# Kernel optimization log

Hardware: AMD Instinct MI355X
Metric: run time of the kernel (lower is better)

The kernel has to match this reference:

```python
import jax, jax.numpy as jnp
import numpy as np

LEVELS = 2
_H0 = jnp.array([0.0322231, -0.01260397, -0.09921954, 0.2978578,
                 0.80373875, 0.49761867, -0.02963553, -0.07576571], dtype=jnp.float32)
_H1 = _H0[::-1] * jnp.array([-1.0, 1.0] * 4, dtype=jnp.float32)  # db4 QMF


def subband_conv2d(x, kernel_2d, stride):
    # depthwise grouped conv: same 2D kernel applied to every channel
    C = x.shape[-1]
    k = jnp.tile(kernel_2d[:, :, None, None], (1, 1, 1, C))  # HWIO with I=1, groups=C
    return jax.lax.conv_general_dilated(
        x, k, window_strides=(stride, stride), padding='SAME',
        dimension_numbers=('NHWC', 'HWIO', 'NHWC'), feature_group_count=C)


def _upsample2d(t):
    B, H, W, C = t.shape
    return jnp.zeros((B, 2 * H, 2 * W, C), t.dtype).at[:, ::2, ::2, :].set(t)


def _local_conv(t, w):
    # per-spatial-position linear map over channels: [B,H,W,I] x [I,O,W,H] -> [B,H,W,O]
    return jnp.einsum('bhwi,iowh->bhwo', t, w)


def setup_inputs() -> dict:
    key = jax.random.key(0)
    ks = jax.random.split(key, 9)
    B, H, W, C, O = 16, 128, 128, 64, 64
    inp = {
        'x': jax.random.normal(ks[0], (B, H, W, C), dtype=jnp.float32),
        'wLL': 0.02 * jax.random.normal(ks[1], (C, O, 32, 32), dtype=jnp.float32),
        'wLH_l0': 0.02 * jax.random.normal(ks[2], (C, O, 64, 64), dtype=jnp.float32),
        'wHL_l0': 0.02 * jax.random.normal(ks[3], (C, O, 64, 64), dtype=jnp.float32),
        'wHH_l0': 0.02 * jax.random.normal(ks[4], (C, O, 64, 64), dtype=jnp.float32),
        'wLH_l1': 0.02 * jax.random.normal(ks[5], (C, O, 32, 32), dtype=jnp.float32),
        'wHL_l1': 0.02 * jax.random.normal(ks[6], (C, O, 32, 32), dtype=jnp.float32),
        'wHH_l1': 0.02 * jax.random.normal(ks[7], (C, O, 32, 32), dtype=jnp.float32),
    }
    return inp


def reference(x, wLL, wLH_l0, wHL_l0, wHH_l0, wLH_l1, wHL_l1, wHH_l1):
    h0, h1 = _H0, _H1
    g0, g1 = h0[::-1], h1[::-1]
    # H=W=128 is divisible by 2**levels, so no symmetric padding is needed.
    res = x
    details = []
    for _ in range(LEVELS):
        cLL = subband_conv2d(res, jnp.outer(h0, h0), 2)
        cLH = subband_conv2d(res, jnp.outer(h0, h1), 2)
        cHL = subband_conv2d(res, jnp.outer(h1, h0), 2)
        cHH = subband_conv2d(res, jnp.outer(h1, h1), 2)
        details.append((cLH, cHL, cHH))
        res = cLL
    yA = _local_conv(res, wLL)  # [B,32,32,O]
    det_w = [(wLH_l0, wHL_l0, wHH_l0), (wLH_l1, wHL_l1, wHH_l1)]
    td = []
    for i in range(LEVELS):
        lh, hl, hh = details[i]
        wlh, whl, whh = det_w[i]
        td.append((_local_conv(lh, wlh), _local_conv(hl, whl), _local_conv(hh, whh)))
    r = yA
    for i in reversed(range(LEVELS)):
        yLH, yHL, yHH = td[i]
        r = (subband_conv2d(_upsample2d(r), jnp.outer(g0, g0), 1)
             + subband_conv2d(_upsample2d(yLH), jnp.outer(g0, g1), 1)
             + subband_conv2d(_upsample2d(yHL), jnp.outer(g1, g0), 1)
             + subband_conv2d(_upsample2d(yHH), jnp.outer(g1, g1), 1))
    return r
```

## Files before the change

### kernel.cpp

```cpp
#include <hip/hip_runtime.h>

__device__ __constant__ float H0[8] = { 0.0322231f, -0.01260397f, -0.09921954f,  0.2978578f,
                                        0.80373875f, 0.49761867f, -0.02963553f, -0.07576571f};
__device__ __constant__ float H1[8] = { 0.07576571f, -0.02963553f, -0.49761867f, 0.80373875f,
                                       -0.2978578f, -0.09921954f,  0.01260397f,  0.0322231f};
__device__ __constant__ float G0[8] = {-0.07576571f, -0.02963553f,  0.49761867f, 0.80373875f,
                                        0.2978578f,  -0.09921954f, -0.01260397f, 0.0322231f};
__device__ __constant__ float G1[8] = { 0.0322231f,   0.01260397f, -0.09921954f, -0.2978578f,
                                        0.80373875f, -0.49761867f, -0.02963553f, 0.07576571f};

template<int HIN>
__global__ __launch_bounds__(256) void fwd_dwt(const float* __restrict__ in,
                                               float* __restrict__ oLL, float* __restrict__ oLH,
                                               float* __restrict__ oHL, float* __restrict__ oHH)
{
    constexpr int OH = HIN / 2;
    constexpr int TQ = OH / 2;
    const int tid = threadIdx.x;
    const int c = tid & 63;
    const int s = blockIdx.x * 4 + (tid >> 6);
    const int j = s % TQ;
    const int i = (s / TQ) % TQ;
    const int b = s / (TQ * TQ);

    float acc[2][2][4];
#pragma unroll
    for (int a = 0; a < 2; ++a)
#pragma unroll
        for (int d = 0; d < 2; ++d)
#pragma unroll
            for (int k = 0; k < 4; ++k) acc[a][d][k] = 0.f;

    const int iw0 = 4 * j - 3;
#pragma unroll
    for (int r = 0; r < 10; ++r) {
        const int ih = 4 * i + r - 3;
        if ((unsigned)ih < (unsigned)HIN) {
            const float* row = in + ((b * HIN + ih) * HIN) * 64 + c;
            float xv[10];
#pragma unroll
            for (int v = 0; v < 10; ++v) {
                const int iw = iw0 + v;
                xv[v] = ((unsigned)iw < (unsigned)HIN) ? row[iw * 64] : 0.f;
            }
            float h00 = 0.f, h01 = 0.f, h10 = 0.f, h11 = 0.f;
#pragma unroll
            for (int v = 0; v < 8; ++v) {
                h00 += H0[v] * xv[v];
                h10 += H1[v] * xv[v];
                h01 += H0[v] * xv[v + 2];
                h11 += H1[v] * xv[v + 2];
            }
#pragma unroll
            for (int ii = 0; ii < 2; ++ii) {
                const int u = r - 2 * ii;
                if (0 <= u && u < 8) {
                    const float a0 = H0[u], a1 = H1[u];
                    acc[ii][0][0] += a0 * h00;
                    acc[ii][0][1] += a0 * h10;
                    acc[ii][0][2] += a1 * h00;
                    acc[ii][0][3] += a1 * h10;
                    acc[ii][1][0] += a0 * h01;
                    acc[ii][1][1] += a0 * h11;
                    acc[ii][1][2] += a1 * h01;
                    acc[ii][1][3] += a1 * h11;
                }
            }
        }
    }

#pragma unroll
    for (int ii = 0; ii < 2; ++ii)
#pragma unroll
        for (int jj = 0; jj < 2; ++jj) {
            const int oh = 2 * i + ii, ow = 2 * j + jj;
            const int oidx = ((b * OH + oh) * OH + ow) * 64 + c;
            oLL[oidx] = acc[ii][jj][0];
            oLH[oidx] = acc[ii][jj][1];
            oHL[oidx] = acc[ii][jj][2];
            oHH[oidx] = acc[ii][jj][3];
        }
}

template<int HD>
__global__ __launch_bounds__(256) void act_tr(const float* __restrict__ in,
                                              float* __restrict__ outp)
{
    __shared__ float Ld[64][HD + 1];
    const int w = blockIdx.x;
    const int b = blockIdx.y;
    const int t = threadIdx.x;

    {
        const int i = t & 63;
        const int hq = t >> 6;
#pragma unroll
        for (int s = 0; s < HD / 4; ++s) {
            const int h = hq * (HD / 4) + s;
            Ld[i][h] = in[((size_t)(b * HD + h) * HD + w) * 64 + i];
        }
    }
    __syncthreads();
    {
        const int h = t & (HD - 1);
        const int iq = t / HD;
        constexpr int NIQ = 256 / HD;
#pragma unroll
        for (int s = 0; s < 64 / NIQ; ++s) {
            const int i = s * NIQ + iq;
            outp[((size_t)(w * 64 + i) * 16 + b) * HD + h] = Ld[i][h];
        }
    }
}

template<int HD, int OT>
__global__ __launch_bounds__(256) void local_conv_v8(
    const float* __restrict__ a0, const float* __restrict__ a1,
    const float* __restrict__ a2, const float* __restrict__ a3,
    const float* __restrict__ w0, const float* __restrict__ w1,
    const float* __restrict__ w2, const float* __restrict__ w3,
    float* __restrict__ o0, float* __restrict__ o1,
    float* __restrict__ o2, float* __restrict__ o3)
{
    constexpr int WH   = HD * HD;
    constexpr int HG   = HD / 32;
    constexpr int OGN  = 64 / OT;
    constexpr int PERZ = OGN * HD * HG;
    constexpr int NB   = 2;
    constexpr int NO4  = OT / 4;
    constexpr int NR   = 8;

    __shared__ float E[NB][32][NO4 * 4 + 4];

    const int nwg = gridDim.x;
    const int hb  = blockIdx.x;
    const int l   = (hb & 7) * (nwg >> 3) + (hb >> 3);

    const int z   = l / PERZ;
    int rem       = l - z * PERZ;
    const int w   = rem / (OGN * HG);
    rem          -= w * (OGN * HG);
    const int og  = rem / HG;
    const int hg  = rem - og * HG;
    const int hbase = hg * 32;

    const float* act = (z == 0) ? a0 : (z == 1) ? a1 : (z == 2) ? a2 : a3;
    const float* wgt = (z == 0) ? w0 : (z == 1) ? w1 : (z == 2) ? w2 : w3;
    float*       out = (z == 0) ? o0 : (z == 1) ? o1 : (z == 2) ? o2 : o3;

    const int t  = threadIdx.x;
    const int hc = t & 31;
    const int r  = t >> 5;
    const int b0 = r * NB;

    const float* wp = wgt + (size_t)(og * OT) * WH + w * HD + hbase + hc;
    const float* ap = act + ((size_t)(w * 64) * 16 + b0) * HD + hbase + hc;

    float acc[NB][OT];
#pragma unroll
    for (int j = 0; j < NB; ++j)
#pragma unroll
        for (int q = 0; q < OT; ++q) acc[j][q] = 0.f;

    for (int ch = 0; ch < 32; ++ch) {
        const int i0 = ch * 2;
        float wr[2][OT];
        float ar[2][NB];
#pragma unroll
        for (int ii = 0; ii < 2; ++ii) {
#pragma unroll
            for (int q = 0; q < OT; ++q)
                wr[ii][q] = wp[(size_t)((i0 + ii) * 64 + q) * WH];
#pragma unroll
            for (int j = 0; j < NB; ++j)
                ar[ii][j] = ap[(size_t)((i0 + ii) * 16 + j) * HD];
        }
#pragma unroll
        for (int ii = 0; ii < 2; ++ii)
#pragma unroll
            for (int j = 0; j < NB; ++j) {
                const float a = ar[ii][j];
#pragma unroll
                for (int q = 0; q < OT; ++q)
                    acc[j][q] += a * wr[ii][q];
            }
    }

    const int oF = t & (NO4 - 1);
    const int h2 = (t / NO4) & 31;
    const int be = t / (NO4 * 32);

    for (int p = 0; p < NR; ++p) {
        if (p) __syncthreads();
        if (r == p) {
#pragma unroll
            for (int j = 0; j < NB; ++j)
#pragma unroll
                for (int q = 0; q < OT; ++q)
                    E[j][hc][q] = acc[j][q];
        }
        __syncthreads();
        if (be < NB) {
            float4 v = *(const float4*)&E[be][h2][oF * 4];
            const int b = p * NB + be;
            *(float4*)(out + ((size_t)(b * HD + hbase + h2) * HD + w) * 64
                       + og * OT + oF * 4) = v;
        }
    }
}

template<int HOUT>
__global__ __launch_bounds__(256) void inv_dwt(const float* __restrict__ yLL,
                                               const float* __restrict__ yLH,
                                               const float* __restrict__ yHL,
                                               const float* __restrict__ yHH,
                                               float* __restrict__ out)
{
    constexpr int HS = HOUT / 2;
    const int tid = threadIdx.x;
    const int c = tid & 63;
    const int s = blockIdx.x * 4 + (tid >> 6);
    const int j = s % HS;
    const int i = (s / HS) % HS;
    const int b = s / (HS * HS);

    float Pe[4] = {0.f, 0.f, 0.f, 0.f}, Po[4] = {0.f, 0.f, 0.f, 0.f};
    float Qe[4] = {0.f, 0.f, 0.f, 0.f}, Qo[4] = {0.f, 0.f, 0.f, 0.f};

#pragma unroll
    for (int ku = 0; ku < 4; ++ku) {
        const int m = i - 1 + ku;
        if ((unsigned)m < (unsigned)HS) {
            const float a0e = G0[1 + 2 * ku], a0o = G0[2 * ku];
            const float a1e = G1[1 + 2 * ku], a1o = G1[2 * ku];
            const int rowoff = (b * HS + m) * HS;
#pragma unroll
            for (int kv = 0; kv < 4; ++kv) {
                const int n = j - 1 + kv;
                if ((unsigned)n < (unsigned)HS) {
                    const int idx = (rowoff + n) * 64 + c;
                    const float yll = yLL[idx], ylh = yLH[idx];
                    const float yhl = yHL[idx], yhh = yHH[idx];
                    Pe[kv] += a0e * yll + a1e * yhl;
                    Po[kv] += a0o * yll + a1o * yhl;
                    Qe[kv] += a0e * ylh + a1e * yhh;
                    Qo[kv] += a0o * ylh + a1o * yhh;
                }
            }
        }
    }

    float o00 = 0.f, o01 = 0.f, o10 = 0.f, o11 = 0.f;
#pragma unroll
    for (int kv = 0; kv < 4; ++kv) {
        const float b0e = G0[1 + 2 * kv], b0o = G0[2 * kv];
        const float b1e = G1[1 + 2 * kv], b1o = G1[2 * kv];
        o00 += b0e * Pe[kv] + b1e * Qe[kv];
        o01 += b0o * Pe[kv] + b1o * Qe[kv];
        o10 += b0e * Po[kv] + b1e * Qo[kv];
        o11 += b0o * Po[kv] + b1o * Qo[kv];
    }

    const int h0 = 2 * i, w0 = 2 * j;
    const int base = ((b * HOUT + h0) * HOUT + w0) * 64 + c;
    out[base] = o00;
    out[base + 64] = o01;
    out[base + HOUT * 64] = o10;
    out[base + HOUT * 64 + 64] = o11;
}

extern "C" void kernel_launch(void* const* d_in, const int* in_sizes, int n_in,
                              void* d_out, int out_size, void* d_ws, size_t ws_size,
                              hipStream_t stream)
{
    const float* x    = (const float*)d_in[0];
    const float* wLL  = (const float*)d_in[1];
    const float* wLH0 = (const float*)d_in[2];
    const float* wHL0 = (const float*)d_in[3];
    const float* wHH0 = (const float*)d_in[4];
    const float* wLH1 = (const float*)d_in[5];
    const float* wHL1 = (const float*)d_in[6];
    const float* wHH1 = (const float*)d_in[7];
    float* out = (float*)d_out;
    float* ws  = (float*)d_ws;

    const int S0 = 16 * 64 * 64 * 64;
    const int S1 = 16 * 32 * 32 * 64;

    float* c0 = out;
    float* A0 = out;
    float* A1 = out + 3 * S0;

    float* c1 = ws;
    float* t0 = ws + 4 * S1;
    float* t1 = ws + 4 * S1 + 3 * S0;
    float* yA = ws + 7 * S1 + 3 * S0;
    float* r1 = ws;

    fwd_dwt<128><<<16 * 32 * 32 / 4, 256, 0, stream>>>(x, c0, c0 + S0, c0 + 2 * S0, c0 + 3 * S0);

    fwd_dwt<64><<<16 * 16 * 16 / 4, 256, 0, stream>>>(c0,
        c1 + 0 * S1, c1 + 1 * S1, c1 + 2 * S1, c1 + 3 * S1);

    act_tr<64><<<dim3(64, 16), 256, 0, stream>>>(c0 + 1 * S0, A0 + 0 * S0);
    act_tr<64><<<dim3(64, 16), 256, 0, stream>>>(c0 + 2 * S0, A0 + 1 * S0);
    act_tr<64><<<dim3(64, 16), 256, 0, stream>>>(c0 + 3 * S0, A0 + 2 * S0);

    act_tr<32><<<dim3(32, 16), 256, 0, stream>>>(c1 + 0 * S1, A1 + 0 * S1);
    act_tr<32><<<dim3(32, 16), 256, 0, stream>>>(c1 + 1 * S1, A1 + 1 * S1);
    act_tr<32><<<dim3(32, 16), 256, 0, stream>>>(c1 + 2 * S1, A1 + 2 * S1);
    act_tr<32><<<dim3(32, 16), 256, 0, stream>>>(c1 + 3 * S1, A1 + 3 * S1);

    local_conv_v8<64, 16><<<1536, 256, 0, stream>>>(
        A0 + 0 * S0, A0 + 1 * S0, A0 + 2 * S0, nullptr,
        wLH0, wHL0, wHH0, nullptr,
        t0 + 0 * S0, t0 + 1 * S0, t0 + 2 * S0, nullptr);

    local_conv_v8<32, 8><<<1024, 256, 0, stream>>>(
        A1 + 1 * S1, A1 + 2 * S1, A1 + 3 * S1, A1 + 0 * S1,
        wLH1, wHL1, wHH1, wLL,
        t1 + 0 * S1, t1 + 1 * S1, t1 + 2 * S1, yA);

    inv_dwt<64><<<16 * 32 * 32 / 4, 256, 0, stream>>>(
        yA, t1 + 0 * S1, t1 + 1 * S1, t1 + 2 * S1, r1);

    inv_dwt<128><<<16 * 64 * 64 / 4, 256, 0, stream>>>(
        r1, t0 + 0 * S0, t0 + 1 * S0, t0 + 2 * S0, out);
}
```

Measured before the change: 357.1 us.

## Retile local conv per output column and store results directly without LDS staging

Measured after the change: 326.3 us. 8.6% less time.

```diff
diff --git a/kernel.cpp b/kernel.cpp
--- a/kernel.cpp
+++ b/kernel.cpp
@@ -113,8 +113,8 @@
     }
 }
 
-template<int HD, int OT>
-__global__ __launch_bounds__(256) void local_conv_v8(
+template<int HD, int OT, int WPB>
+__global__ __launch_bounds__(256) void local_conv_v9(
     const float* __restrict__ a0, const float* __restrict__ a1,
     const float* __restrict__ a2, const float* __restrict__ a3,
     const float* __restrict__ w0, const float* __restrict__ w1,
@@ -123,38 +123,33 @@
     float* __restrict__ o2, float* __restrict__ o3)
 {
     constexpr int WH   = HD * HD;
-    constexpr int HG   = HD / 32;
     constexpr int OGN  = 64 / OT;
-    constexpr int PERZ = OGN * HD * HG;
-    constexpr int NB   = 2;
-    constexpr int NO4  = OT / 4;
-    constexpr int NR   = 8;
-
-    __shared__ float E[NB][32][NO4 * 4 + 4];
+    constexpr int WPN  = HD / WPB;
+    constexpr int PERZ = WPN * OGN;
+    constexpr int NB   = 4;
 
     const int nwg = gridDim.x;
     const int hb  = blockIdx.x;
     const int l   = (hb & 7) * (nwg >> 3) + (hb >> 3);
 
     const int z   = l / PERZ;
-    int rem       = l - z * PERZ;
-    const int w   = rem / (OGN * HG);
-    rem          -= w * (OGN * HG);
-    const int og  = rem / HG;
-    const int hg  = rem - og * HG;
-    const int hbase = hg * 32;
+    const int rem = l - z * PERZ;
+    const int wp  = rem / OGN;
+    const int og  = rem - wp * OGN;
 
     const float* act = (z == 0) ? a0 : (z == 1) ? a1 : (z == 2) ? a2 : a3;
     const float* wgt = (z == 0) ? w0 : (z == 1) ? w1 : (z == 2) ? w2 : w3;
     float*       out = (z == 0) ? o0 : (z == 1) ? o1 : (z == 2) ? o2 : o3;
 
     const int t  = threadIdx.x;
-    const int hc = t & 31;
-    const int r  = t >> 5;
+    const int hc = t % HD;
+    const int wq = (t / HD) % WPB;
+    const int r  = t / (HD * WPB);
     const int b0 = r * NB;
-
-    const float* wp = wgt + (size_t)(og * OT) * WH + w * HD + hbase + hc;
-    const float* ap = act + ((size_t)(w * 64) * 16 + b0) * HD + hbase + hc;
+    const int wbase = wp * WPB + wq;
+
+    const float* wpp = wgt + (size_t)(og * OT) * WH + wbase * HD + hc;
+    const float* ap  = act + ((size_t)(wbase * 64) * 16 + b0) * HD + hc;
 
     float acc[NB][OT];
 #pragma unroll
@@ -170,7 +165,7 @@
         for (int ii = 0; ii < 2; ++ii) {
 #pragma unroll
             for (int q = 0; q < OT; ++q)
-                wr[ii][q] = wp[(size_t)((i0 + ii) * 64 + q) * WH];
+                wr[ii][q] = wpp[(size_t)((i0 + ii) * 64 + q) * WH];
 #pragma unroll
             for (int j = 0; j < NB; ++j)
                 ar[ii][j] = ap[(size_t)((i0 + ii) * 16 + j) * HD];
@@ -186,25 +181,15 @@
             }
     }
 
-    const int oF = t & (NO4 - 1);
-    const int h2 = (t / NO4) & 31;
-    const int be = t / (NO4 * 32);
-
-    for (int p = 0; p < NR; ++p) {
-        if (p) __syncthreads();
-        if (r == p) {
-#pragma unroll
-            for (int j = 0; j < NB; ++j)
-#pragma unroll
-                for (int q = 0; q < OT; ++q)
-                    E[j][hc][q] = acc[j][q];
-        }
-        __syncthreads();
-        if (be < NB) {
-            float4 v = *(const float4*)&E[be][h2][oF * 4];
-            const int b = p * NB + be;
-            *(float4*)(out + ((size_t)(b * HD + hbase + h2) * HD + w) * 64
-                       + og * OT + oF * 4) = v;
+#pragma unroll
+    for (int j = 0; j < NB; ++j) {
+        const int b = b0 + j;
+        float* op = out + ((size_t)(b * HD + hc) * HD + wbase) * 64 + og * OT;
+#pragma unroll
+        for (int q4 = 0; q4 < OT / 4; ++q4) {
+            float4 v = make_float4(acc[j][q4 * 4 + 0], acc[j][q4 * 4 + 1],
+                                   acc[j][q4 * 4 + 2], acc[j][q4 * 4 + 3]);
+            *(float4*)(op + q4 * 4) = v;
         }
     }
 }
@@ -311,12 +296,12 @@
     act_tr<32><<<dim3(32, 16), 256, 0, stream>>>(c1 + 2 * S1, A1 + 2 * S1);
     act_tr<32><<<dim3(32, 16), 256, 0, stream>>>(c1 + 3 * S1, A1 + 3 * S1);
 
-    local_conv_v8<64, 16><<<1536, 256, 0, stream>>>(
+    local_conv_v9<64, 8, 1><<<1536, 256, 0, stream>>>(
         A0 + 0 * S0, A0 + 1 * S0, A0 + 2 * S0, nullptr,
         wLH0, wHL0, wHH0, nullptr,
         t0 + 0 * S0, t0 + 1 * S0, t0 + 2 * S0, nullptr);
 
-    local_conv_v8<32, 8><<<1024, 256, 0, stream>>>(
+    local_conv_v9<32, 4, 2><<<1024, 256, 0, stream>>>(
         A1 + 1 * S1, A1 + 2 * S1, A1 + 3 * S1, A1 + 0 * S1,
         wLH1, wHL1, wHH1, wLL,
         t1 + 0 * S1, t1 + 1 * S1, t1 + 2 * S1, yA);
```
